# Optimization experiments

Hardware: AMD Instinct MI355X
Metric: run time of the kernel (lower is better)

The kernel has to match this reference:

```python
import jax, jax.numpy as jnp
import numpy as np

B, N, C = 8, 2_000_000, 16


def _per_batch_loss(x, t, num_classes):
    """x: [N] float values, t: [N] int labels.
    For each label group: loss = mean(group) - mode(group) (scipy mode,
    ties -> smallest value), scattered back to every position of that label.
    """
    n = x.shape[0]
    # Sort primarily by label, secondarily by value (lexsort: last key primary).
    order = jnp.lexsort((x, t))
    xs = x[order]
    ts = t[order]
    # Run-length encode equal (label, value) pairs to count value multiplicity.
    new_run = jnp.concatenate(
        [jnp.ones((1,), bool), (ts[1:] != ts[:-1]) | (xs[1:] != xs[:-1])])
    run_id = jnp.cumsum(new_run) - 1                      # [N]
    run_cnt = jax.ops.segment_sum(jnp.ones(n, xs.dtype), run_id,
                                  num_segments=n)[run_id]  # count per element
    # Mode per label = smallest value attaining the max multiplicity.
    grp_max = jax.ops.segment_max(run_cnt, ts, num_segments=num_classes)
    mode = jax.ops.segment_min(
        jnp.where(run_cnt == grp_max[ts], xs, jnp.inf), ts,
        num_segments=num_classes)                         # [C]
    ssum = jax.ops.segment_sum(xs, ts, num_segments=num_classes)
    scnt = jax.ops.segment_sum(jnp.ones(n, xs.dtype), ts,
                               num_segments=num_classes)
    mean = ssum / jnp.maximum(scnt, 1.0)
    per_label = jnp.where(scnt > 0, mean - mode, 0.0)     # [C]
    return per_label[t]                                    # scatter back, [N]


def setup_inputs() -> dict:
    key = jax.random.key(0)
    k1, k2 = jax.random.split(key)
    inputs = jax.random.normal(k1, (B, N), dtype=jnp.float32)
    targets = jax.random.randint(k2, (B, N), 0, C, dtype=jnp.int32)
    return {"inputs": inputs, "targets": targets, "num_classes": C}


def reference(inputs, targets, num_classes):
    per_pos = jax.vmap(lambda x, t: _per_batch_loss(x, t, num_classes))(
        inputs, targets)                                   # [B, N]
    return jnp.mean(per_pos)
```

## Files before the change

kernel.cpp:

```cpp
#include <hip/hip_runtime.h>
#include <stdint.h>

#define NUM_C 16
#define NUM_B 8
#define NBKT (NUM_C * 64)
#define NGRP 256
#define CHUNK_S 8192
#define TAB 4096
#define MODE_CAP 3072
#define MAX_NB 8

__device__ __forceinline__ unsigned hash_u32(unsigned h) {
    h ^= h >> 16; h *= 0x85ebca6bu;
    h ^= h >> 13; h *= 0xc2b2ae35u;
    h ^= h >> 16;
    return h;
}
__device__ __forceinline__ unsigned canon_key(float v) {
    unsigned k = __float_as_uint(v);
    return (k == 0x80000000u) ? 0u : k;
}
__device__ __forceinline__ unsigned bucket_of(unsigned key, int c) {
    return ((unsigned)c << 6) | (hash_u32(key) >> 26);
}

__global__ void __launch_bounds__(512)
sort_kernel(const float* __restrict__ x, const int* __restrict__ t,
            long long N, int bbase, int nchunk, int nchpad,
            unsigned* __restrict__ keysout, unsigned short* __restrict__ offsT)
{
    __shared__ unsigned hist[NBKT];
    __shared__ unsigned lout[CHUNK_S];
    __shared__ unsigned wsum[8];
    const int lb = blockIdx.x / nchunk;
    const int ch = blockIdx.x % nchunk;
    const int b  = bbase + lb;
    const long long base = (long long)ch * CHUNK_S;
    const int count = (int)((N - base < CHUNK_S) ? (N - base) : CHUNK_S);
    const float* xb = x + (size_t)b * N + base;
    const int*   tb = t + (size_t)b * N + base;
    const int tid = threadIdx.x;

    for (int i = tid; i < NBKT; i += 512) hist[i] = 0u;
    __syncthreads();

    unsigned keys[16], pk[16];
    const int n4 = count >> 2;
    #pragma unroll
    for (int r = 0; r < 4; ++r) {
        const int idx4 = tid + r * 512;
        if (idx4 < n4) {
            float4 v  = ((const float4*)xb)[idx4];
            int4   cc = ((const int4*)tb)[idx4];
            unsigned k0 = canon_key(v.x), b0 = bucket_of(k0, cc.x);
            unsigned k1 = canon_key(v.y), b1 = bucket_of(k1, cc.y);
            unsigned k2 = canon_key(v.z), b2 = bucket_of(k2, cc.z);
            unsigned k3 = canon_key(v.w), b3 = bucket_of(k3, cc.w);
            unsigned p0 = atomicAdd(&hist[b0], 1u);
            unsigned p1 = atomicAdd(&hist[b1], 1u);
            unsigned p2 = atomicAdd(&hist[b2], 1u);
            unsigned p3 = atomicAdd(&hist[b3], 1u);
            keys[r*4+0] = k0; pk[r*4+0] = (b0 << 13) | p0;
            keys[r*4+1] = k1; pk[r*4+1] = (b1 << 13) | p1;
            keys[r*4+2] = k2; pk[r*4+2] = (b2 << 13) | p2;
            keys[r*4+3] = k3; pk[r*4+3] = (b3 << 13) | p3;
        }
    }
    unsigned kex = 0u, pkx = 0u; int hex = 0;
    {
        const int remi = (n4 << 2) + tid;
        if (remi < count) {
            unsigned k = canon_key(xb[remi]);
            unsigned bk = bucket_of(k, tb[remi]);
            unsigned p = atomicAdd(&hist[bk], 1u);
            kex = k; pkx = (bk << 13) | p; hex = 1;
        }
    }
    __syncthreads();

    {
        unsigned b0v = hist[2 * tid], b1v = hist[2 * tid + 1];
        unsigned s = b0v + b1v, inc = s;
        const int lane = tid & 63;
        #pragma unroll
        for (int d = 1; d < 64; d <<= 1) {
            unsigned tt = __shfl_up(inc, d);
            if (lane >= d) inc += tt;
        }
        if (lane == 63) wsum[tid >> 6] = inc;
        __syncthreads();
        unsigned wbase = 0;
        for (int i = 0; i < (tid >> 6); ++i) wbase += wsum[i];
        unsigned excl = wbase + inc - s;
        hist[2 * tid]     = excl + b0v;
        hist[2 * tid + 1] = excl + s;
        __syncthreads();
    }

    #pragma unroll
    for (int r = 0; r < 4; ++r) {
        const int idx4 = tid + r * 512;
        if (idx4 < n4) {
            #pragma unroll
            for (int c2 = 0; c2 < 4; ++c2) {
                unsigned bk = pk[r*4+c2] >> 13, p = pk[r*4+c2] & 8191u;
                lout[(bk ? hist[bk - 1] : 0u) + p] = keys[r*4+c2];
            }
        }
    }
    if (hex) {
        unsigned bk = pkx >> 13, p = pkx & 8191u;
        lout[(bk ? hist[bk - 1] : 0u) + p] = kex;
    }
    __syncthreads();

    unsigned* kb = keysout + (size_t)lb * N + base;
    if (count == CHUNK_S) {
        #pragma unroll
        for (int r = 0; r < 4; ++r)
            ((uint4*)kb)[tid + r * 512] = ((const uint4*)lout)[tid + r * 512];
    } else {
        for (int i = tid; i < count; i += 512) kb[i] = lout[i];
    }
    unsigned short* ocol = offsT + (size_t)lb * 1025 * nchpad + ch;
    ocol[(size_t)tid * nchpad] = (unsigned short)(tid ? hist[tid - 1] : 0u);
    ocol[(size_t)(tid + 512) * nchpad] = (unsigned short)hist[tid + 511];
    if (tid == 0) ocol[(size_t)1024 * nchpad] = (unsigned short)hist[1023];
}

__global__ void __launch_bounds__(512)
mode_kernel(const unsigned* __restrict__ keysout,
            const unsigned short* __restrict__ offsT,
            long long N, int nchunk, int nchpad, int bbase,
            unsigned long long* __restrict__ best,
            double* __restrict__ psum,
            unsigned* __restrict__ pcnt)
{
    __shared__ unsigned keyt[TAB];
    __shared__ unsigned cnt16[TAB / 2];
    __shared__ unsigned staging[4][MODE_CAP];
    __shared__ unsigned short rowbuf[5][256];
    __shared__ unsigned short pos[4][256];
    __shared__ unsigned tot[4];
    __shared__ unsigned long long redb[8];
    __shared__ double reds[8];

    const unsigned nwg = gridDim.x;
    const unsigned logical = (blockIdx.x & 7u) * (nwg >> 3) + (blockIdx.x >> 3);
    const unsigned lb = logical >> 8;
    const unsigned G  = logical & 255u;
    const unsigned g0 = G << 2;
    const unsigned c  = G >> 4;
    const unsigned b  = (unsigned)bbase + lb;
    const int tid = threadIdx.x;
    const int lane = tid & 63, wid = tid >> 6;

    const uint4 z4 = make_uint4(0u, 0u, 0u, 0u);
    for (int i = tid; i < TAB / 4; i += 512) ((uint4*)keyt)[i] = z4;
    for (int i = tid; i < TAB / 8; i += 512) ((uint4*)cnt16)[i] = z4;

    const unsigned short* obT = offsT + (size_t)lb * 1025 * nchpad;
    for (int i = tid; i < 5 * 256; i += 512) {
        int r = i >> 8, q = i & 255;
        rowbuf[r][q] = (q < nchunk)
            ? obT[(size_t)(g0 + r) * nchpad + q] : (unsigned short)0;
    }
    __syncthreads();

    if (wid < 4) {
        const int sb = wid;
        unsigned lpre[4], run = 0;
        #pragma unroll
        for (int k = 0; k < 4; ++k) {
            int q = lane * 4 + k;
            lpre[k] = run;
            run += (unsigned)rowbuf[sb + 1][q] - (unsigned)rowbuf[sb][q];
        }
        unsigned inc = run;
        #pragma unroll
        for (int d = 1; d < 64; d <<= 1) {
            unsigned tt = __shfl_up(inc, d);
            if (lane >= d) inc += tt;
        }
        unsigned basex = inc - run;
        #pragma unroll
        for (int k = 0; k < 4; ++k)
            pos[sb][lane * 4 + k] = (unsigned short)(basex + lpre[k]);
        if (lane == 63) tot[sb] = inc;
    }
    __syncthreads();

    const unsigned* kb = keysout + (size_t)lb * N;
    double ls = 0.0;
    unsigned mo = 0xFFFFFFFFu;

    const int sub = lane >> 4, j = lane & 15;
    const int nit = (nchunk + 31) >> 5;
    for (int it = 0; it < nit; ++it) {
        int q = it * 32 + wid * 4 + sub;
        if (q < nchunk) {
            unsigned s0 = rowbuf[0][q];
            unsigned rb1 = (unsigned)rowbuf[1][q] - s0;
            unsigned rb2 = (unsigned)rowbuf[2][q] - s0;
            unsigned rb3 = (unsigned)rowbuf[3][q] - s0;
            unsigned len = (unsigned)rowbuf[4][q] - s0;
            const unsigned* src = kb + (size_t)q * CHUNK_S + s0;
            for (unsigned jj = (unsigned)j; jj < len; jj += 16u) {
                unsigned key = src[jj];
                ls += (double)__uint_as_float(key);
                unsigned o = (key & 0x80000000u) ? ~key : (key | 0x80000000u);
                if (o < mo) mo = o;
                int sb = (jj >= rb2) ? ((jj >= rb3) ? 3 : 2)
                                     : ((jj >= rb1) ? 1 : 0);
                unsigned rel = jj - (sb == 0 ? 0u : (sb == 1 ? rb1
                                    : (sb == 2 ? rb2 : rb3)));
                unsigned dst = (unsigned)pos[sb][q] + rel;
                if (dst < MODE_CAP) staging[sb][dst] = o;
            }
        }
    }
    __syncthreads();

    unsigned bc = 0u, bo = 0xFFFFFFFFu;
    for (int sb = 0; sb < 4; ++sb) {
        unsigned n = tot[sb]; if (n > MODE_CAP) n = MODE_CAP;
        const unsigned* stg = staging[sb];
        for (unsigned base0 = 0; base0 < n; base0 += 2048u) {
            unsigned od[4], h[4], old[4];
            int nv = 0;
            #pragma unroll
            for (int k = 0; k < 4; ++k) {
                unsigned idx = base0 + (unsigned)tid + (unsigned)k * 512u;
                if (idx < n) {
                    unsigned o = stg[idx];
                    od[k] = o; h[k] = hash_u32(o) & (TAB - 1);
                    nv = k + 1;
                }
            }
            #pragma unroll
            for (int k = 0; k < 4; ++k)
                if (k < nv) old[k] = atomicCAS(&keyt[h[k]], 0u, od[k]);
            #pragma unroll
            for (int k = 0; k < 4; ++k) {
                if (k >= nv) continue;
                unsigned o = old[k], hh = h[k];
                const unsigned oo = od[k];
                unsigned cnt = 1u;
                while (o != 0u) {
                    if (o == oo) {
                        unsigned sh = (hh & 1u) << 4;
                        unsigned ret = atomicAdd(&cnt16[hh >> 1], 1u << sh);
                        cnt = ((ret >> sh) & 0xFFFFu) + 2u;
                        break;
                    }
                    hh = (hh + 1u) & (TAB - 1u);
                    o = atomicCAS(&keyt[hh], 0u, oo);
                }
                if (cnt >= 2u && (cnt > bc || (cnt == bc && oo < bo))) {
                    bc = cnt; bo = oo;
                }
            }
        }
        if (sb < 3) {
            __syncthreads();
            for (int i = tid; i < TAB / 4; i += 512) ((uint4*)keyt)[i] = z4;
            for (int i = tid; i < TAB / 8; i += 512) ((uint4*)cnt16)[i] = z4;
            __syncthreads();
        }
    }

    unsigned long long lbst = bc ? (((unsigned long long)bc << 32)
                                    | (unsigned long long)(~bo)) : 0ull;
    {
        unsigned long long s1 = (1ull << 32) | (unsigned long long)(~mo);
        if (s1 > lbst) lbst = s1;
    }
    #pragma unroll
    for (int sh = 32; sh > 0; sh >>= 1) {
        unsigned long long obv = __shfl_down(lbst, sh);
        if (obv > lbst) lbst = obv;
        ls += __shfl_down(ls, sh);
    }
    if (lane == 0) { redb[wid] = lbst; reds[wid] = ls; }
    __syncthreads();
    if (tid == 0) {
        unsigned long long bb = 0ull; double ss = 0.0;
        #pragma unroll
        for (int i = 0; i < 8; ++i) {
            if (redb[i] > bb) bb = redb[i];
            ss += reds[i];
        }
        psum[b * NGRP + G] = ss;
        pcnt[b * NGRP + G] = tot[0] + tot[1] + tot[2] + tot[3];
        if (bb) atomicMax(&best[b * NUM_C + c], bb);
    }
}

__global__ void __launch_bounds__(128)
finalize_kernel(const double* __restrict__ psum,
                const unsigned* __restrict__ pcnt,
                const unsigned long long* __restrict__ best,
                float* __restrict__ out, double inv_total)
{
    __shared__ double acc[NUM_B * NUM_C];
    const int i = threadIdx.x;
    const int b = i >> 4, c = i & 15;

    double s = 0.0;
    unsigned long long cnt = 0ull;
    const double*   ps = psum + (size_t)b * NGRP + ((size_t)c << 4);
    const unsigned* pc = pcnt + (size_t)b * NGRP + ((size_t)c << 4);
    for (int r = 0; r < 16; ++r) { s += ps[r]; cnt += pc[r]; }

    double term = 0.0;
    if (cnt > 0ull) {
        unsigned long long p = best[i];
        unsigned ord = 0xFFFFFFFFu - (unsigned)(p & 0xFFFFFFFFull);
        unsigned ub  = (ord & 0x80000000u) ? (ord ^ 0x80000000u) : ~ord;
        float mode = __uint_as_float(ub);
        term = s - (double)cnt * (double)mode;
    }
    acc[i] = term;
    __syncthreads();
    for (int st = 64; st > 0; st >>= 1) {
        if (i < st) acc[i] += acc[i + st];
        __syncthreads();
    }
    if (i == 0) out[0] = (float)(acc[0] * inv_total);
}

extern "C" void kernel_launch(void* const* d_in, const int* in_sizes, int n_in,
                              void* d_out, int out_size, void* d_ws, size_t ws_size,
                              hipStream_t stream)
{
    const float* x = (const float*)d_in[0];
    const int*   t = (const int*)d_in[1];

    const long long total = in_sizes[0];
    const long long N = total / NUM_B;
    const int nchunk = (int)((N + CHUNK_S - 1) / CHUNK_S);
    const int nchpad = (nchunk + 63) & ~63;

    char* ws = (char*)d_ws;
    size_t off = 0;
    unsigned long long* best = (unsigned long long*)(ws + off);
    off += (size_t)NUM_B * NUM_C * 8;
    double* psum = (double*)(ws + off);
    off += (size_t)NUM_B * NGRP * 8;
    unsigned* pcnt = (unsigned*)(ws + off);
    off += (size_t)NUM_B * NGRP * 4;
    off = (off + 255) & ~(size_t)255;

    const size_t keys_per_b = (size_t)N * 4;
    const size_t offs_per_b = (size_t)1025 * nchpad * 2;
    const size_t per_b = keys_per_b + offs_per_b + 512;
    size_t remaining = ws_size - off;
    int nb = (int)(remaining / per_b);
    if (nb < 1) nb = 1;
    if (nb > MAX_NB) nb = MAX_NB;
    {
        int rounds = (NUM_B + nb - 1) / nb;
        nb = (NUM_B + rounds - 1) / rounds;
    }

    unsigned* keysout = (unsigned*)(ws + off);
    off += (size_t)nb * keys_per_b;
    off = (off + 255) & ~(size_t)255;
    unsigned short* offsT = (unsigned short*)(ws + off);
    off += (size_t)nb * offs_per_b;

    hipMemsetAsync(best, 0, (size_t)NUM_B * NUM_C * 8, stream);
    for (int r = 0; r < NUM_B; r += nb) {
        const int nbr = (NUM_B - r < nb) ? (NUM_B - r) : nb;
        sort_kernel<<<nbr * nchunk, 512, 0, stream>>>(
            x, t, N, r, nchunk, nchpad, keysout, offsT);
        mode_kernel<<<nbr * NGRP, 512, 0, stream>>>(
            keysout, offsT, N, nchunk, nchpad, r, best, psum, pcnt);
    }
    finalize_kernel<<<1, 128, 0, stream>>>(
        psum, pcnt, best, (float*)d_out,
        1.0 / ((double)NUM_B * (double)N));
}
```

Baseline: 299.6 us.

## Halve sort chunk, transpose offsets separately, hash directly from global keys

Sort chunks shrink from 8192 to 4096 keys, which doubles the number of sort blocks and halves the register and LDS use of each. Per-chunk bucket offsets are now written row-contiguously and moved into the column layout by a new tiled transpose kernel, replacing the scattered strided short writes. The mode kernel drops the LDS staging buffer and prefix-scan pass and inserts keys into the hash table straight from global memory, with element counts accumulated by reduction. This removes the MODE_CAP truncation and one LDS pass, at the cost of an extra kernel launch, more chunks to iterate, and a narrower loop of 4 lanes per chunk that may issue less efficient global loads.

```diff
diff --git a/kernel.cpp b/kernel.cpp
--- a/kernel.cpp
+++ b/kernel.cpp
@@ -5,9 +5,8 @@
 #define NUM_B 8
 #define NBKT (NUM_C * 64)
 #define NGRP 256
-#define CHUNK_S 8192
+#define CHUNK_S 4096
 #define TAB 4096
-#define MODE_CAP 3072
 #define MAX_NB 8
 
 __device__ __forceinline__ unsigned hash_u32(unsigned h) {
@@ -26,8 +25,8 @@
 
 __global__ void __launch_bounds__(512)
 sort_kernel(const float* __restrict__ x, const int* __restrict__ t,
-            long long N, int bbase, int nchunk, int nchpad,
-            unsigned* __restrict__ keysout, unsigned short* __restrict__ offsT)
+            long long N, int bbase, int nchunk,
+            unsigned* __restrict__ keysout, unsigned short* __restrict__ offs)
 {
     __shared__ unsigned hist[NBKT];
     __shared__ unsigned lout[CHUNK_S];
@@ -44,10 +43,10 @@
     for (int i = tid; i < NBKT; i += 512) hist[i] = 0u;
     __syncthreads();
 
-    unsigned keys[16], pk[16];
+    unsigned keys[8], pk[8];
     const int n4 = count >> 2;
     #pragma unroll
-    for (int r = 0; r < 4; ++r) {
+    for (int r = 0; r < 2; ++r) {
         const int idx4 = tid + r * 512;
         if (idx4 < n4) {
             float4 v  = ((const float4*)xb)[idx4];
@@ -98,7 +97,7 @@
     }
 
     #pragma unroll
-    for (int r = 0; r < 4; ++r) {
+    for (int r = 0; r < 2; ++r) {
         const int idx4 = tid + r * 512;
         if (idx4 < n4) {
             #pragma unroll
@@ -117,15 +116,45 @@
     unsigned* kb = keysout + (size_t)lb * N + base;
     if (count == CHUNK_S) {
         #pragma unroll
-        for (int r = 0; r < 4; ++r)
+        for (int r = 0; r < 2; ++r)
             ((uint4*)kb)[tid + r * 512] = ((const uint4*)lout)[tid + r * 512];
     } else {
         for (int i = tid; i < count; i += 512) kb[i] = lout[i];
     }
-    unsigned short* ocol = offsT + (size_t)lb * 1025 * nchpad + ch;
-    ocol[(size_t)tid * nchpad] = (unsigned short)(tid ? hist[tid - 1] : 0u);
-    ocol[(size_t)(tid + 512) * nchpad] = (unsigned short)hist[tid + 511];
-    if (tid == 0) ocol[(size_t)1024 * nchpad] = (unsigned short)hist[1023];
+    unsigned short* orow = offs + ((size_t)lb * nchunk + ch) * 1025;
+    orow[tid]       = (unsigned short)(tid ? hist[tid - 1] : 0u);
+    orow[tid + 512] = (unsigned short)hist[tid + 511];
+    if (tid == 0) orow[1024] = (unsigned short)hist[1023];
+}
+
+__global__ void __launch_bounds__(256)
+transpose_kernel(const unsigned short* __restrict__ offs,
+                 unsigned short* __restrict__ offsT, int nchunk, int nchpad)
+{
+    __shared__ unsigned short tile[32][33];
+    const int tiles_r = 33;
+    const int tiles_c = (nchunk + 31) >> 5;
+    const int lb  = blockIdx.x / (tiles_r * tiles_c);
+    const int rem = blockIdx.x % (tiles_r * tiles_c);
+    const int r0 = (rem / tiles_c) * 32;
+    const int c0 = (rem % tiles_c) * 32;
+    const unsigned short* src = offs + (size_t)lb * nchunk * 1025;
+    unsigned short* dst = offsT + (size_t)lb * 1025 * nchpad;
+    const int tx = threadIdx.x & 31, ty = threadIdx.x >> 5;
+
+    #pragma unroll
+    for (int dy = 0; dy < 32; dy += 8) {
+        int ch = c0 + ty + dy, row = r0 + tx;
+        tile[ty + dy][tx] = (ch < nchunk && row < 1025)
+            ? src[(size_t)ch * 1025 + row] : (unsigned short)0;
+    }
+    __syncthreads();
+    #pragma unroll
+    for (int dy = 0; dy < 32; dy += 8) {
+        int row = r0 + ty + dy, ch = c0 + tx;
+        if (row < 1025 && ch < nchpad)
+            dst[(size_t)row * nchpad + ch] = tile[tx][ty + dy];
+    }
 }
 
 __global__ void __launch_bounds__(512)
@@ -138,12 +167,10 @@
 {
     __shared__ unsigned keyt[TAB];
     __shared__ unsigned cnt16[TAB / 2];
-    __shared__ unsigned staging[4][MODE_CAP];
-    __shared__ unsigned short rowbuf[5][256];
-    __shared__ unsigned short pos[4][256];
-    __shared__ unsigned tot[4];
+    __shared__ unsigned short rowbuf[5][512];
     __shared__ unsigned long long redb[8];
     __shared__ double reds[8];
+    __shared__ unsigned redc[8];
 
     const unsigned nwg = gridDim.x;
     const unsigned logical = (blockIdx.x & 7u) * (nwg >> 3) + (blockIdx.x >> 3);
@@ -160,104 +187,51 @@
     for (int i = tid; i < TAB / 8; i += 512) ((uint4*)cnt16)[i] = z4;
 
     const unsigned short* obT = offsT + (size_t)lb * 1025 * nchpad;
-    for (int i = tid; i < 5 * 256; i += 512) {
-        int r = i >> 8, q = i & 255;
+    for (int i = tid; i < 5 * 512; i += 512) {
+        int r = i >> 9, q = i & 511;
         rowbuf[r][q] = (q < nchunk)
             ? obT[(size_t)(g0 + r) * nchpad + q] : (unsigned short)0;
-    }
-    __syncthreads();
-
-    if (wid < 4) {
-        const int sb = wid;
-        unsigned lpre[4], run = 0;
-        #pragma unroll
-        for (int k = 0; k < 4; ++k) {
-            int q = lane * 4 + k;
-            lpre[k] = run;
-            run += (unsigned)rowbuf[sb + 1][q] - (unsigned)rowbuf[sb][q];
-        }
-        unsigned inc = run;
-        #pragma unroll
-        for (int d = 1; d < 64; d <<= 1) {
-            unsigned tt = __shfl_up(inc, d);
-            if (lane >= d) inc += tt;
-        }
-        unsigned basex = inc - run;
-        #pragma unroll
-        for (int k = 0; k < 4; ++k)
-            pos[sb][lane * 4 + k] = (unsigned short)(basex + lpre[k]);
-        if (lane == 63) tot[sb] = inc;
     }
     __syncthreads();
 
     const unsigned* kb = keysout + (size_t)lb * N;
     double ls = 0.0;
     unsigned mo = 0xFFFFFFFFu;
-
-    const int sub = lane >> 4, j = lane & 15;
-    const int nit = (nchunk + 31) >> 5;
-    for (int it = 0; it < nit; ++it) {
-        int q = it * 32 + wid * 4 + sub;
-        if (q < nchunk) {
-            unsigned s0 = rowbuf[0][q];
-            unsigned rb1 = (unsigned)rowbuf[1][q] - s0;
-            unsigned rb2 = (unsigned)rowbuf[2][q] - s0;
-            unsigned rb3 = (unsigned)rowbuf[3][q] - s0;
-            unsigned len = (unsigned)rowbuf[4][q] - s0;
-            const unsigned* src = kb + (size_t)q * CHUNK_S + s0;
-            for (unsigned jj = (unsigned)j; jj < len; jj += 16u) {
-                unsigned key = src[jj];
-                ls += (double)__uint_as_float(key);
-                unsigned o = (key & 0x80000000u) ? ~key : (key | 0x80000000u);
-                if (o < mo) mo = o;
-                int sb = (jj >= rb2) ? ((jj >= rb3) ? 3 : 2)
-                                     : ((jj >= rb1) ? 1 : 0);
-                unsigned rel = jj - (sb == 0 ? 0u : (sb == 1 ? rb1
-                                    : (sb == 2 ? rb2 : rb3)));
-                unsigned dst = (unsigned)pos[sb][q] + rel;
-                if (dst < MODE_CAP) staging[sb][dst] = o;
-            }
-        }
-    }
-    __syncthreads();
-
+    unsigned lc = 0u;
     unsigned bc = 0u, bo = 0xFFFFFFFFu;
+
+    const int nit = (nchunk + 127) >> 7;
     for (int sb = 0; sb < 4; ++sb) {
-        unsigned n = tot[sb]; if (n > MODE_CAP) n = MODE_CAP;
-        const unsigned* stg = staging[sb];
-        for (unsigned base0 = 0; base0 < n; base0 += 2048u) {
-            unsigned od[4], h[4], old[4];
-            int nv = 0;
-            #pragma unroll
-            for (int k = 0; k < 4; ++k) {
-                unsigned idx = base0 + (unsigned)tid + (unsigned)k * 512u;
-                if (idx < n) {
-                    unsigned o = stg[idx];
-                    od[k] = o; h[k] = hash_u32(o) & (TAB - 1);
-                    nv = k + 1;
-                }
-            }
-            #pragma unroll
-            for (int k = 0; k < 4; ++k)
-                if (k < nv) old[k] = atomicCAS(&keyt[h[k]], 0u, od[k]);
-            #pragma unroll
-            for (int k = 0; k < 4; ++k) {
-                if (k >= nv) continue;
-                unsigned o = old[k], hh = h[k];
-                const unsigned oo = od[k];
-                unsigned cnt = 1u;
-                while (o != 0u) {
-                    if (o == oo) {
-                        unsigned sh = (hh & 1u) << 4;
-                        unsigned ret = atomicAdd(&cnt16[hh >> 1], 1u << sh);
-                        cnt = ((ret >> sh) & 0xFFFFu) + 2u;
-                        break;
+        for (int it = 0; it < nit; ++it) {
+            const int q = it * 128 + wid * 16 + (lane >> 2);
+            if (q < nchunk) {
+                const unsigned s = rowbuf[sb][q];
+                const unsigned e = rowbuf[sb + 1][q];
+                const unsigned* src = kb + (size_t)q * CHUNK_S;
+                for (unsigned jj = s + (unsigned)(lane & 3); jj < e; jj += 4u) {
+                    unsigned key = src[jj];
+                    ls += (double)__uint_as_float(key);
+                    ++lc;
+                    unsigned o = (key & 0x80000000u) ? ~key
+                                                     : (key | 0x80000000u);
+                    if (o < mo) mo = o;
+                    unsigned hh = hash_u32(o) & (TAB - 1);
+                    unsigned old = atomicCAS(&keyt[hh], 0u, o);
+                    unsigned cnt = 1u;
+                    while (old != 0u) {
+                        if (old == o) {
+                            unsigned sh = (hh & 1u) << 4;
+                            unsigned ret =
+                                atomicAdd(&cnt16[hh >> 1], 1u << sh);
+                            cnt = ((ret >> sh) & 0xFFFFu) + 2u;
+                            break;
+                        }
+                        hh = (hh + 1u) & (TAB - 1u);
+                        old = atomicCAS(&keyt[hh], 0u, o);
                     }
-                    hh = (hh + 1u) & (TAB - 1u);
-                    o = atomicCAS(&keyt[hh], 0u, oo);
-                }
-                if (cnt >= 2u && (cnt > bc || (cnt == bc && oo < bo))) {
-                    bc = cnt; bo = oo;
+                    if (cnt >= 2u && (cnt > bc || (cnt == bc && o < bo))) {
+                        bc = cnt; bo = o;
+                    }
                 }
             }
         }
@@ -280,18 +254,20 @@
         unsigned long long obv = __shfl_down(lbst, sh);
         if (obv > lbst) lbst = obv;
         ls += __shfl_down(ls, sh);
-    }
-    if (lane == 0) { redb[wid] = lbst; reds[wid] = ls; }
+        lc += __shfl_down(lc, sh);
+    }
+    if (lane == 0) { redb[wid] = lbst; reds[wid] = ls; redc[wid] = lc; }
     __syncthreads();
     if (tid == 0) {
-        unsigned long long bb = 0ull; double ss = 0.0;
+        unsigned long long bb = 0ull; double ss = 0.0; unsigned cc = 0u;
         #pragma unroll
         for (int i = 0; i < 8; ++i) {
             if (redb[i] > bb) bb = redb[i];
             ss += reds[i];
+            cc += redc[i];
         }
         psum[b * NGRP + G] = ss;
-        pcnt[b * NGRP + G] = tot[0] + tot[1] + tot[2] + tot[3];
+        pcnt[b * NGRP + G] = cc;
         if (bb) atomicMax(&best[b * NUM_C + c], bb);
     }
 }
@@ -351,9 +327,10 @@
     off += (size_t)NUM_B * NGRP * 4;
     off = (off + 255) & ~(size_t)255;
 
-    const size_t keys_per_b = (size_t)N * 4;
-    const size_t offs_per_b = (size_t)1025 * nchpad * 2;
-    const size_t per_b = keys_per_b + offs_per_b + 512;
+    const size_t keys_per_b  = (size_t)N * 4;
+    const size_t offs_per_b  = (size_t)nchunk * 1025 * 2;
+    const size_t offsT_per_b = (size_t)1025 * nchpad * 2;
+    const size_t per_b = keys_per_b + offs_per_b + offsT_per_b + 512;
     size_t remaining = ws_size - off;
     int nb = (int)(remaining / per_b);
     if (nb < 1) nb = 1;
@@ -366,14 +343,20 @@
     unsigned* keysout = (unsigned*)(ws + off);
     off += (size_t)nb * keys_per_b;
     off = (off + 255) & ~(size_t)255;
+    unsigned short* offsA = (unsigned short*)(ws + off);
+    off += (size_t)nb * offs_per_b;
+    off = (off + 255) & ~(size_t)255;
     unsigned short* offsT = (unsigned short*)(ws + off);
-    off += (size_t)nb * offs_per_b;
-
+    off += (size_t)nb * offsT_per_b;
+
+    const int tiles = 33 * ((nchunk + 31) >> 5);
     hipMemsetAsync(best, 0, (size_t)NUM_B * NUM_C * 8, stream);
     for (int r = 0; r < NUM_B; r += nb) {
         const int nbr = (NUM_B - r < nb) ? (NUM_B - r) : nb;
         sort_kernel<<<nbr * nchunk, 512, 0, stream>>>(
-            x, t, N, r, nchunk, nchpad, keysout, offsT);
+            x, t, N, r, nchunk, keysout, offsA);
+        transpose_kernel<<<nbr * tiles, 256, 0, stream>>>(
+            offsA, offsT, nchunk, nchpad);
         mode_kernel<<<nbr * NGRP, 512, 0, stream>>>(
             keysout, offsT, N, nchunk, nchpad, r, best, psum, pcnt);
     }
```

After: 276.6 us. 7.7% less time.
